# Performance work log

Hardware: AMD Instinct MI355X
Metric: run time of the kernel (lower is better)

Reference implementation:

```python
import jax, jax.numpy as jnp
import numpy as np

B, T, CODE_NUM, MED_NUM = 256, 32, 4880, 1000
CODE_SIZE, H, OUT = 128, 128, 4880


def setup_inputs() -> dict:
    key = jax.random.key(0)
    ks = jax.random.split(key, 16)
    code_x = (jax.random.uniform(ks[0], (B, T, CODE_NUM)) < 0.05).astype(jnp.float32)
    medicine_codes = (jax.random.uniform(ks[1], (B, T, MED_NUM)) < 0.02).astype(jnp.float32)
    divided = (jax.random.uniform(ks[2], (B, T, CODE_NUM)) < 0.05).astype(jnp.float32)
    neighbors = (jax.random.uniform(ks[3], (B, T, CODE_NUM)) < 0.05).astype(jnp.float32)
    lens = jax.random.randint(ks[4], (B,), 1, T + 1)
    s = lambda fan: 1.0 / np.sqrt(fan)
    c_emb = jax.random.normal(ks[5], (CODE_NUM, CODE_SIZE)) * s(CODE_SIZE)
    m_emb = jax.random.normal(ks[6], (MED_NUM, CODE_SIZE)) * s(CODE_SIZE)
    W_c = jax.random.normal(ks[7], (CODE_SIZE, H)) * s(CODE_SIZE)
    W_m = jax.random.normal(ks[8], (CODE_SIZE, H)) * s(CODE_SIZE)
    Wa = jax.random.normal(ks[9], (3 * H, 32)) * s(3 * H)
    ba = jnp.zeros((32,), jnp.float32)
    va = jax.random.normal(ks[10], (32,)) * s(32)
    W_cls = jax.random.normal(ks[11], (3 * H, OUT)) * s(3 * H)
    b_cls = jnp.zeros((OUT,), jnp.float32)
    return dict(code_x=code_x, divided=divided, neighbors=neighbors, lens=lens,
                medicine_codes=medicine_codes, c_emb=c_emb, m_emb=m_emb,
                W_c=W_c, W_m=W_m, Wa=Wa, ba=ba, va=va, W_cls=W_cls, b_cls=b_cls)


def _forward(code_x, medicine_codes, lens, c_emb, m_emb, W_c, W_m, Wa, ba, va, W_cls, b_cls):
    # hypergraph_part: transform code/med embeddings, aggregate active codes per visit
    Hc = jnp.tanh(c_emb @ W_c)                      # [code_num, H]
    Hm = jnp.tanh(m_emb @ W_m)                      # [med_num, H]
    sum_c = jnp.einsum('btc,ch->bth', code_x, Hc)   # masked sum over active dx codes
    sum_m = jnp.einsum('btm,mh->bth', medicine_codes, Hm)
    h_c = sum_c / jnp.clip(code_x.sum(-1, keepdims=True), 1.0, None)
    h_m = sum_m / jnp.clip(medicine_codes.sum(-1, keepdims=True), 1.0, None)
    repre = jnp.concatenate([h_c, h_m, h_c * h_m], axis=-1)  # [B,T,3H]
    # DotProductAttention over visits, masked by lens
    scores = jnp.einsum('btk,k->bt', jnp.tanh(repre @ Wa + ba), va)
    mask = jnp.arange(T)[None, :] < lens[:, None]
    attn = jax.nn.softmax(jnp.where(mask, scores, -1e9), axis=-1)
    ctx = jnp.einsum('bt,btd->bd', attn, repre)     # [B,3H]
    # Classifier (dropout=identity in eval) + sigmoid
    return jax.nn.sigmoid(ctx @ W_cls + b_cls)      # [B,OUT]


def reference(code_x, divided, neighbors, lens, medicine_codes, c_emb, m_emb,
              W_c, W_m, Wa, ba, va, W_cls, b_cls):
    # divided/neighbors feed the transition branch whose output is unused
    # in the original forward's final prediction path.
    return _forward(code_x, medicine_codes, lens, c_emb, m_emb,
                    W_c, W_m, Wa, ba, va, W_cls, b_cls)
```

## Files before the change

kernel.cpp:

```cpp
#include <hip/hip_runtime.h>
#include <hip/hip_bf16.h>
#include <math.h>

#define Bsz 256
#define Tn 32
#define CODEN 4880
#define MEDN 1000
#define Hdim 128
#define OUTN 4880
#define BT (Bsz*Tn)
#define R3H 384

__global__ __launch_bounds__(128) void k_emb(
    const float* __restrict__ c_emb, const float* __restrict__ m_emb,
    const float* __restrict__ W_c, const float* __restrict__ W_m,
    float* __restrict__ Hc, float* __restrict__ Hm) {
  int row = blockIdx.x;
  const float* emb; const float* W; float* out;
  if (row < CODEN) { emb = c_emb + (size_t)row * Hdim; W = W_c; out = Hc + (size_t)row * Hdim; }
  else { int r = row - CODEN; emb = m_emb + (size_t)r * Hdim; W = W_m; out = Hm + (size_t)r * Hdim; }
  __shared__ float e[Hdim];
  int h = threadIdx.x;
  e[h] = emb[h];
  __syncthreads();
  float acc = 0.f;
#pragma unroll 8
  for (int k = 0; k < Hdim; ++k) acc += e[k] * W[k * Hdim + h];
  out[h] = tanhf(acc);
}

#define MAXC 1024
#define MAXM 256

__global__ __launch_bounds__(256) void k_visit(
    const float* __restrict__ code_x, const float* __restrict__ med,
    const float* __restrict__ Hc, const float* __restrict__ Hm,
    const float* __restrict__ Wa, const float* __restrict__ ba,
    const float* __restrict__ va,
    float* __restrict__ repre, float* __restrict__ scores) {
  int bt = blockIdx.x;
  int tid = threadIdx.x;
  __shared__ int list_c[MAXC];
  __shared__ int list_m[MAXM];
  __shared__ int cnt_c, cnt_m;
  __shared__ float rep_s[R3H];
  __shared__ float red[256];
  if (tid == 0) { cnt_c = 0; cnt_m = 0; }
  __syncthreads();

  const float4* cx = (const float4*)(code_x + (size_t)bt * CODEN);
  for (int i = tid; i < CODEN / 4; i += 256) {
    float4 v = cx[i];
    if (v.x != 0.f) { int p = atomicAdd(&cnt_c, 1); if (p < MAXC) list_c[p] = 4*i; }
    if (v.y != 0.f) { int p = atomicAdd(&cnt_c, 1); if (p < MAXC) list_c[p] = 4*i+1; }
    if (v.z != 0.f) { int p = atomicAdd(&cnt_c, 1); if (p < MAXC) list_c[p] = 4*i+2; }
    if (v.w != 0.f) { int p = atomicAdd(&cnt_c, 1); if (p < MAXC) list_c[p] = 4*i+3; }
  }
  const float4* mx = (const float4*)(med + (size_t)bt * MEDN);
  for (int i = tid; i < MEDN / 4; i += 256) {
    float4 v = mx[i];
    if (v.x != 0.f) { int p = atomicAdd(&cnt_m, 1); if (p < MAXM) list_m[p] = 4*i; }
    if (v.y != 0.f) { int p = atomicAdd(&cnt_m, 1); if (p < MAXM) list_m[p] = 4*i+1; }
    if (v.z != 0.f) { int p = atomicAdd(&cnt_m, 1); if (p < MAXM) list_m[p] = 4*i+2; }
    if (v.w != 0.f) { int p = atomicAdd(&cnt_m, 1); if (p < MAXM) list_m[p] = 4*i+3; }
  }
  __syncthreads();
  int nc = cnt_c < MAXC ? cnt_c : MAXC;
  int nm = cnt_m < MAXM ? cnt_m : MAXM;

  int h = tid & 127, half = tid >> 7;
  float accC = 0.f;
#pragma unroll 2
  for (int j = half; j < nc; j += 2) accC += Hc[(size_t)list_c[j] * Hdim + h];
  float accM = 0.f;
#pragma unroll 2
  for (int j = half; j < nm; j += 2) accM += Hm[(size_t)list_m[j] * Hdim + h];

  red[tid] = accC;
  __syncthreads();
  float hc = 0.f, hm = 0.f;
  if (half == 0) hc = (red[h] + red[h + 128]) / fmaxf((float)nc, 1.f);
  __syncthreads();
  red[tid] = accM;
  __syncthreads();
  if (half == 0) {
    hm = (red[h] + red[h + 128]) / fmaxf((float)nm, 1.f);
    rep_s[h] = hc;
    rep_s[Hdim + h] = hm;
    rep_s[2 * Hdim + h] = hc * hm;
  }
  __syncthreads();

  float* rp = repre + (size_t)bt * R3H;
  for (int i = tid; i < R3H; i += 256) rp[i] = rep_s[i];

  int j = tid & 31, kc = tid >> 5;
  float p = 0.f;
  int k0 = kc * 48;
#pragma unroll 8
  for (int k = k0; k < k0 + 48; ++k) p += rep_s[k] * Wa[k * 32 + j];
  __syncthreads();
  red[tid] = p;
  __syncthreads();
  if (tid < 32) {
    float tot = 0.f;
#pragma unroll
    for (int c = 0; c < 8; ++c) tot += red[c * 32 + tid];
    float u = tanhf(tot + ba[tid]);
    float sv = u * va[tid];
#pragma unroll
    for (int off = 16; off >= 1; off >>= 1) sv += __shfl_down(sv, off, 32);
    if (tid == 0) scores[bt] = sv;
  }
}

__global__ __launch_bounds__(128) void k_ctx(
    const float* __restrict__ scores, const int* __restrict__ lens,
    const float* __restrict__ repre, float* __restrict__ ctx) {
  int b = blockIdx.x, tid = threadIdx.x;
  __shared__ float attn[Tn];
  int len = lens[b];
  if (tid < Tn) {
    float s = scores[b * Tn + tid];
    bool valid = tid < len;
    float sm = valid ? s : -1e30f;
    float m = sm;
#pragma unroll
    for (int off = 16; off >= 1; off >>= 1) m = fmaxf(m, __shfl_xor(m, off, 32));
    float e = valid ? expf(sm - m) : 0.f;
    float sum = e;
#pragma unroll
    for (int off = 16; off >= 1; off >>= 1) sum += __shfl_xor(sum, off, 32);
    attn[tid] = e / sum;
  }
  __syncthreads();
  const float* rp = repre + (size_t)b * Tn * R3H;
  for (int d = tid; d < R3H; d += 128) {
    float a = 0.f;
#pragma unroll
    for (int t = 0; t < Tn; ++t) a += attn[t] * rp[t * R3H + d];
    ctx[(size_t)b * R3H + d] = a;
  }
}

#define FMA4(A, s, w) { A.x += (s)*(w).x; A.y += (s)*(w).y; A.z += (s)*(w).z; A.w += (s)*(w).w; }

__global__ __launch_bounds__(256) void k_cls(
    const float* __restrict__ ctx, const float* __restrict__ W_cls,
    const float* __restrict__ b_cls, float* __restrict__ out) {
  __shared__ float cs_t[R3H * 8];
  int tid = threadIdx.x;
  int ob = blockIdx.x % 5;
  int b0 = (blockIdx.x / 5) * 8;
  for (int i = tid; i < R3H * 8; i += 256) {
    int k = i >> 3, r = i & 7;
    cs_t[i] = ctx[(size_t)(b0 + r) * R3H + k];
  }
  __syncthreads();
  int o0 = ob * 1024 + tid * 4;
  if (o0 >= OUTN) return;
  float4 acc[8];
#pragma unroll
  for (int r = 0; r < 8; ++r) acc[r] = make_float4(0.f, 0.f, 0.f, 0.f);
  const float* wp = W_cls + o0;
#pragma unroll 2
  for (int k = 0; k < R3H; ++k) {
    float4 w = *(const float4*)(wp + (size_t)k * OUTN);
    float4 cA = *(const float4*)&cs_t[k * 8];
    float4 cB = *(const float4*)&cs_t[k * 8 + 4];
    FMA4(acc[0], cA.x, w); FMA4(acc[1], cA.y, w);
    FMA4(acc[2], cA.z, w); FMA4(acc[3], cA.w, w);
    FMA4(acc[4], cB.x, w); FMA4(acc[5], cB.y, w);
    FMA4(acc[6], cB.z, w); FMA4(acc[7], cB.w, w);
  }
  float4 bc = *(const float4*)(b_cls + o0);
#pragma unroll
  for (int r = 0; r < 8; ++r) {
    float4 v;
    v.x = 1.f / (1.f + expf(-(acc[r].x + bc.x)));
    v.y = 1.f / (1.f + expf(-(acc[r].y + bc.y)));
    v.z = 1.f / (1.f + expf(-(acc[r].z + bc.z)));
    v.w = 1.f / (1.f + expf(-(acc[r].w + bc.w)));
    *(float4*)(out + (size_t)(b0 + r) * OUTN + o0) = v;
  }
}

extern "C" void kernel_launch(void* const* d_in, const int* in_sizes, int n_in,
                              void* d_out, int out_size, void* d_ws, size_t ws_size,
                              hipStream_t stream) {
  const float* code_x = (const float*)d_in[0];
  const int*   lens   = (const int*)d_in[3];
  const float* med    = (const float*)d_in[4];
  const float* c_emb  = (const float*)d_in[5];
  const float* m_emb  = (const float*)d_in[6];
  const float* W_c    = (const float*)d_in[7];
  const float* W_m    = (const float*)d_in[8];
  const float* Wa     = (const float*)d_in[9];
  const float* ba     = (const float*)d_in[10];
  const float* va     = (const float*)d_in[11];
  const float* W_cls  = (const float*)d_in[12];
  const float* b_cls  = (const float*)d_in[13];
  float* out = (float*)d_out;
  float* ws  = (float*)d_ws;

  float* Hc     = ws;
  float* Hm     = ws + 624640;
  float* repre  = ws + 752640;
  float* scores = ws + 3898368;
  float* ctx    = ws + 3906560;

  hipLaunchKernelGGL(k_emb,   dim3(CODEN + MEDN), dim3(128), 0, stream,
                     c_emb, m_emb, W_c, W_m, Hc, Hm);
  hipLaunchKernelGGL(k_visit, dim3(BT), dim3(256), 0, stream,
                     code_x, med, Hc, Hm, Wa, ba, va, repre, scores);
  hipLaunchKernelGGL(k_ctx,   dim3(Bsz), dim3(128), 0, stream,
                     scores, lens, repre, ctx);
  hipLaunchKernelGGL(k_cls,   dim3(160), dim3(256), 0, stream,
                     ctx, W_cls, b_cls, out);
}
```

Measured before the change: 606.5 us.

## Store Hc/Hm as bf16 pairs, compact with wave ballots, batch classifier loads

Hc and Hm are now written as packed bf16 pairs, halving the bytes read by the per-visit gather, which is now spread over four wavefront groups. Index-list compaction replaces per-element shared atomics with wave ballots plus mbcnt prefix offsets and one atomic per wave. The classifier loop issues eight weight loads before consuming them to give more memory-level parallelism. The bf16 storage lowers precision of the aggregated embeddings, and the list order changes, which perturbs summation order.

```diff
diff --git a/kernel.cpp b/kernel.cpp
--- a/kernel.cpp
+++ b/kernel.cpp
@@ -10,15 +10,27 @@
 #define OUTN 4880
 #define BT (Bsz*Tn)
 #define R3H 384
+#define NC4 (CODEN/4)
+#define NM4 (MEDN/4)
+
+__device__ inline int mbcnt64(unsigned long long m) {
+  return __builtin_amdgcn_mbcnt_hi((unsigned)(m >> 32),
+         __builtin_amdgcn_mbcnt_lo((unsigned)m, 0));
+}
+
+__device__ inline unsigned f2bf(float f) {
+  unsigned u = __float_as_uint(f);
+  return (u + 0x7fffu + ((u >> 16) & 1u)) >> 16;
+}
 
 __global__ __launch_bounds__(128) void k_emb(
     const float* __restrict__ c_emb, const float* __restrict__ m_emb,
     const float* __restrict__ W_c, const float* __restrict__ W_m,
-    float* __restrict__ Hc, float* __restrict__ Hm) {
+    unsigned* __restrict__ Hc2, unsigned* __restrict__ Hm2) {
   int row = blockIdx.x;
-  const float* emb; const float* W; float* out;
-  if (row < CODEN) { emb = c_emb + (size_t)row * Hdim; W = W_c; out = Hc + (size_t)row * Hdim; }
-  else { int r = row - CODEN; emb = m_emb + (size_t)r * Hdim; W = W_m; out = Hm + (size_t)r * Hdim; }
+  const float* emb; const float* W; unsigned* out2;
+  if (row < CODEN) { emb = c_emb + (size_t)row * Hdim; W = W_c; out2 = Hc2 + (size_t)row * 64; }
+  else { int r = row - CODEN; emb = m_emb + (size_t)r * Hdim; W = W_m; out2 = Hm2 + (size_t)r * 64; }
   __shared__ float e[Hdim];
   int h = threadIdx.x;
   e[h] = emb[h];
@@ -26,7 +38,9 @@
   float acc = 0.f;
 #pragma unroll 8
   for (int k = 0; k < Hdim; ++k) acc += e[k] * W[k * Hdim + h];
-  out[h] = tanhf(acc);
+  float vme = tanhf(acc);
+  float vnx = __shfl_down(vme, 1, 64);
+  if ((h & 1) == 0) out2[h >> 1] = f2bf(vme) | (f2bf(vnx) << 16);
 }
 
 #define MAXC 1024
@@ -34,60 +48,98 @@
 
 __global__ __launch_bounds__(256) void k_visit(
     const float* __restrict__ code_x, const float* __restrict__ med,
-    const float* __restrict__ Hc, const float* __restrict__ Hm,
+    const unsigned* __restrict__ Hc2, const unsigned* __restrict__ Hm2,
     const float* __restrict__ Wa, const float* __restrict__ ba,
     const float* __restrict__ va,
     float* __restrict__ repre, float* __restrict__ scores) {
   int bt = blockIdx.x;
   int tid = threadIdx.x;
+  int lane = tid & 63;
   __shared__ int list_c[MAXC];
   __shared__ int list_m[MAXM];
   __shared__ int cnt_c, cnt_m;
   __shared__ float rep_s[R3H];
-  __shared__ float red[256];
+  __shared__ float red[512];
   if (tid == 0) { cnt_c = 0; cnt_m = 0; }
   __syncthreads();
 
   const float4* cx = (const float4*)(code_x + (size_t)bt * CODEN);
-  for (int i = tid; i < CODEN / 4; i += 256) {
-    float4 v = cx[i];
-    if (v.x != 0.f) { int p = atomicAdd(&cnt_c, 1); if (p < MAXC) list_c[p] = 4*i; }
-    if (v.y != 0.f) { int p = atomicAdd(&cnt_c, 1); if (p < MAXC) list_c[p] = 4*i+1; }
-    if (v.z != 0.f) { int p = atomicAdd(&cnt_c, 1); if (p < MAXC) list_c[p] = 4*i+2; }
-    if (v.w != 0.f) { int p = atomicAdd(&cnt_c, 1); if (p < MAXC) list_c[p] = 4*i+3; }
-  }
-  const float4* mx = (const float4*)(med + (size_t)bt * MEDN);
-  for (int i = tid; i < MEDN / 4; i += 256) {
-    float4 v = mx[i];
-    if (v.x != 0.f) { int p = atomicAdd(&cnt_m, 1); if (p < MAXM) list_m[p] = 4*i; }
-    if (v.y != 0.f) { int p = atomicAdd(&cnt_m, 1); if (p < MAXM) list_m[p] = 4*i+1; }
-    if (v.z != 0.f) { int p = atomicAdd(&cnt_m, 1); if (p < MAXM) list_m[p] = 4*i+2; }
-    if (v.w != 0.f) { int p = atomicAdd(&cnt_m, 1); if (p < MAXM) list_m[p] = 4*i+3; }
+#pragma unroll
+  for (int it = 0; it < 5; ++it) {
+    int i = it * 256 + tid;
+    float4 v = make_float4(0.f, 0.f, 0.f, 0.f);
+    if (i < NC4) v = cx[i];
+    unsigned long long m0 = __ballot(v.x != 0.f);
+    unsigned long long m1 = __ballot(v.y != 0.f);
+    unsigned long long m2 = __ballot(v.z != 0.f);
+    unsigned long long m3 = __ballot(v.w != 0.f);
+    int c0 = __popcll(m0), c1 = __popcll(m1), c2 = __popcll(m2), c3 = __popcll(m3);
+    int base = 0;
+    if (lane == 0) base = atomicAdd(&cnt_c, c0 + c1 + c2 + c3);
+    base = __builtin_amdgcn_readfirstlane(base);
+    int p;
+    p = base + mbcnt64(m0);           if (v.x != 0.f && p < MAXC) list_c[p] = 4*i;
+    p = base + c0 + mbcnt64(m1);      if (v.y != 0.f && p < MAXC) list_c[p] = 4*i+1;
+    p = base + c0+c1 + mbcnt64(m2);   if (v.z != 0.f && p < MAXC) list_c[p] = 4*i+2;
+    p = base + c0+c1+c2 + mbcnt64(m3);if (v.w != 0.f && p < MAXC) list_c[p] = 4*i+3;
+  }
+  {
+    const float4* mx = (const float4*)(med + (size_t)bt * MEDN);
+    int i = tid;
+    float4 v = make_float4(0.f, 0.f, 0.f, 0.f);
+    if (i < NM4) v = mx[i];
+    unsigned long long m0 = __ballot(v.x != 0.f);
+    unsigned long long m1 = __ballot(v.y != 0.f);
+    unsigned long long m2 = __ballot(v.z != 0.f);
+    unsigned long long m3 = __ballot(v.w != 0.f);
+    int c0 = __popcll(m0), c1 = __popcll(m1), c2 = __popcll(m2), c3 = __popcll(m3);
+    int base = 0;
+    if (lane == 0) base = atomicAdd(&cnt_m, c0 + c1 + c2 + c3);
+    base = __builtin_amdgcn_readfirstlane(base);
+    int p;
+    p = base + mbcnt64(m0);           if (v.x != 0.f && p < MAXM) list_m[p] = 4*i;
+    p = base + c0 + mbcnt64(m1);      if (v.y != 0.f && p < MAXM) list_m[p] = 4*i+1;
+    p = base + c0+c1 + mbcnt64(m2);   if (v.z != 0.f && p < MAXM) list_m[p] = 4*i+2;
+    p = base + c0+c1+c2 + mbcnt64(m3);if (v.w != 0.f && p < MAXM) list_m[p] = 4*i+3;
   }
   __syncthreads();
   int nc = cnt_c < MAXC ? cnt_c : MAXC;
   int nm = cnt_m < MAXM ? cnt_m : MAXM;
 
-  int h = tid & 127, half = tid >> 7;
-  float accC = 0.f;
-#pragma unroll 2
-  for (int j = half; j < nc; j += 2) accC += Hc[(size_t)list_c[j] * Hdim + h];
-  float accM = 0.f;
-#pragma unroll 2
-  for (int j = half; j < nm; j += 2) accM += Hm[(size_t)list_m[j] * Hdim + h];
-
-  red[tid] = accC;
+  int g = tid >> 6, t = lane;
+  float aCx = 0.f, aCy = 0.f;
+#pragma unroll 4
+  for (int j = g; j < nc; j += 4) {
+    unsigned v = Hc2[(size_t)list_c[j] * 64 + t];
+    aCx += __uint_as_float(v << 16);
+    aCy += __uint_as_float(v & 0xffff0000u);
+  }
+  float aMx = 0.f, aMy = 0.f;
+#pragma unroll 4
+  for (int j = g; j < nm; j += 4) {
+    unsigned v = Hm2[(size_t)list_m[j] * 64 + t];
+    aMx += __uint_as_float(v << 16);
+    aMy += __uint_as_float(v & 0xffff0000u);
+  }
+
+  red[g * 128 + 2 * t]     = aCx;
+  red[g * 128 + 2 * t + 1] = aCy;
   __syncthreads();
   float hc = 0.f, hm = 0.f;
-  if (half == 0) hc = (red[h] + red[h + 128]) / fmaxf((float)nc, 1.f);
-  __syncthreads();
-  red[tid] = accM;
-  __syncthreads();
-  if (half == 0) {
-    hm = (red[h] + red[h + 128]) / fmaxf((float)nm, 1.f);
-    rep_s[h] = hc;
-    rep_s[Hdim + h] = hm;
-    rep_s[2 * Hdim + h] = hc * hm;
+  if (tid < 128) {
+    float s = red[tid] + red[128 + tid] + red[256 + tid] + red[384 + tid];
+    hc = s / fmaxf((float)nc, 1.f);
+  }
+  __syncthreads();
+  red[g * 128 + 2 * t]     = aMx;
+  red[g * 128 + 2 * t + 1] = aMy;
+  __syncthreads();
+  if (tid < 128) {
+    float s = red[tid] + red[128 + tid] + red[256 + tid] + red[384 + tid];
+    hm = s / fmaxf((float)nm, 1.f);
+    rep_s[tid]             = hc;
+    rep_s[Hdim + tid]      = hm;
+    rep_s[2 * Hdim + tid]  = hc * hm;
   }
   __syncthreads();
 
@@ -95,12 +147,12 @@
   for (int i = tid; i < R3H; i += 256) rp[i] = rep_s[i];
 
   int j = tid & 31, kc = tid >> 5;
-  float p = 0.f;
+  float pacc = 0.f;
   int k0 = kc * 48;
 #pragma unroll 8
-  for (int k = k0; k < k0 + 48; ++k) p += rep_s[k] * Wa[k * 32 + j];
-  __syncthreads();
-  red[tid] = p;
+  for (int k = k0; k < k0 + 48; ++k) pacc += rep_s[k] * Wa[k * 32 + j];
+  __syncthreads();
+  red[tid] = pacc;
   __syncthreads();
   if (tid < 32) {
     float tot = 0.f;
@@ -143,7 +195,9 @@
   }
 }
 
-#define FMA4(A, s, w) { A.x += (s)*(w).x; A.y += (s)*(w).y; A.z += (s)*(w).z; A.w += (s)*(w).w; }
+__device__ inline void fma4(float4& a, float s, const float4& w) {
+  a.x += s * w.x; a.y += s * w.y; a.z += s * w.z; a.w += s * w.w;
+}
 
 __global__ __launch_bounds__(256) void k_cls(
     const float* __restrict__ ctx, const float* __restrict__ W_cls,
@@ -163,15 +217,19 @@
 #pragma unroll
   for (int r = 0; r < 8; ++r) acc[r] = make_float4(0.f, 0.f, 0.f, 0.f);
   const float* wp = W_cls + o0;
-#pragma unroll 2
-  for (int k = 0; k < R3H; ++k) {
-    float4 w = *(const float4*)(wp + (size_t)k * OUTN);
-    float4 cA = *(const float4*)&cs_t[k * 8];
-    float4 cB = *(const float4*)&cs_t[k * 8 + 4];
-    FMA4(acc[0], cA.x, w); FMA4(acc[1], cA.y, w);
-    FMA4(acc[2], cA.z, w); FMA4(acc[3], cA.w, w);
-    FMA4(acc[4], cB.x, w); FMA4(acc[5], cB.y, w);
-    FMA4(acc[6], cB.z, w); FMA4(acc[7], cB.w, w);
+  for (int k = 0; k < R3H; k += 8) {
+    float4 wv[8];
+#pragma unroll
+    for (int u = 0; u < 8; ++u) wv[u] = *(const float4*)(wp + (size_t)(k + u) * OUTN);
+#pragma unroll
+    for (int u = 0; u < 8; ++u) {
+      float4 cA = *(const float4*)&cs_t[(k + u) * 8];
+      float4 cB = *(const float4*)&cs_t[(k + u) * 8 + 4];
+      fma4(acc[0], cA.x, wv[u]); fma4(acc[1], cA.y, wv[u]);
+      fma4(acc[2], cA.z, wv[u]); fma4(acc[3], cA.w, wv[u]);
+      fma4(acc[4], cB.x, wv[u]); fma4(acc[5], cB.y, wv[u]);
+      fma4(acc[6], cB.z, wv[u]); fma4(acc[7], cB.w, wv[u]);
+    }
   }
   float4 bc = *(const float4*)(b_cls + o0);
 #pragma unroll
@@ -203,16 +261,16 @@
   float* out = (float*)d_out;
   float* ws  = (float*)d_ws;
 
-  float* Hc     = ws;
-  float* Hm     = ws + 624640;
-  float* repre  = ws + 752640;
-  float* scores = ws + 3898368;
-  float* ctx    = ws + 3906560;
+  unsigned* Hc2    = (unsigned*)ws;
+  unsigned* Hm2    = (unsigned*)ws + 312320;
+  float*    repre  = ws + 376320;
+  float*    scores = ws + 3522048;
+  float*    ctx    = ws + 3530240;
 
   hipLaunchKernelGGL(k_emb,   dim3(CODEN + MEDN), dim3(128), 0, stream,
-                     c_emb, m_emb, W_c, W_m, Hc, Hm);
+                     c_emb, m_emb, W_c, W_m, Hc2, Hm2);
   hipLaunchKernelGGL(k_visit, dim3(BT), dim3(256), 0, stream,
-                     code_x, med, Hc, Hm, Wa, ba, va, repre, scores);
+                     code_x, med, Hc2, Hm2, Wa, ba, va, repre, scores);
   hipLaunchKernelGGL(k_ctx,   dim3(Bsz), dim3(128), 0, stream,
                      scores, lens, repre, ctx);
   hipLaunchKernelGGL(k_cls,   dim3(160), dim3(256), 0, stream,
```

Measured after the change: 535.8 us. 11.6% less time.
